# Optimization experiments

Measured on AMD Instinct MI355X. Metric: run time of the kernel, lower is better.

The kernel has to match this reference:

```python
import jax, jax.numpy as jnp
import numpy as np

B, C, HD, H, W = 4, 64, 64, 64, 64  # batch, input_dim, hidden_dim, spatial


def conv1x1(x, w, b):
    # x: [B, Cin, H, W], w: [Cout, Cin], b: [Cout]
    return jnp.einsum('oc,bchw->bohw', w, x) + b[None, :, None, None]


def setup_inputs() -> dict:
    key = jax.random.key(0)
    ks = jax.random.split(key, 16)
    sc = lambda cin: 1.0 / np.sqrt(cin)
    d = {
        'h': jax.random.normal(ks[0], (B, C, H, W), jnp.float32),
        'm': jax.random.normal(ks[1], (B, C, H, W), jnp.float32),
        'Wq': jax.random.normal(ks[2], (HD, C), jnp.float32) * sc(C),
        'bq': jnp.zeros((HD,), jnp.float32),
        'Wk': jax.random.normal(ks[3], (HD, C), jnp.float32) * sc(C),
        'bk': jnp.zeros((HD,), jnp.float32),
        'Wk2': jax.random.normal(ks[4], (HD, C), jnp.float32) * sc(C),
        'bk2': jnp.zeros((HD,), jnp.float32),
        'Wv': jax.random.normal(ks[5], (C, C), jnp.float32) * sc(C),
        'bv': jnp.zeros((C,), jnp.float32),
        'Wv2': jax.random.normal(ks[6], (C, C), jnp.float32) * sc(C),
        'bv2': jnp.zeros((C,), jnp.float32),
        'Wz': jax.random.normal(ks[7], (2 * C, 2 * C), jnp.float32) * sc(2 * C),
        'bz': jnp.zeros((2 * C,), jnp.float32),
        'Wm': jax.random.normal(ks[8], (3 * C, 3 * C), jnp.float32) * sc(3 * C),
        'bm': jnp.zeros((3 * C,), jnp.float32),
    }
    return d


def reference(h, m, Wq, bq, Wk, bk, Wk2, bk2, Wv, bv, Wv2, bv2, Wz, bz, Wm, bm):
    b, c, hh, ww = h.shape
    n = hh * ww
    K_h = conv1x1(h, Wk, bk).reshape(b, HD, n)            # [B, HD, N]
    Q_h = conv1x1(h, Wq, bq).reshape(b, HD, n).transpose(0, 2, 1)  # [B, N, HD]
    V_h = conv1x1(h, Wv, bv).reshape(b, c, n)             # [B, C, N]
    K_m = conv1x1(m, Wk2, bk2).reshape(b, HD, n)
    V_m = conv1x1(m, Wv2, bv2).reshape(b, c, n)

    A_h = jax.nn.softmax(jnp.einsum('bnd,bdk->bnk', Q_h, K_h), axis=-1)  # [B, N, N]
    Z_h = jnp.einsum('bnk,bck->bcn', A_h, V_h).reshape(b, c, hh, ww)
    A_m = jax.nn.softmax(jnp.einsum('bnd,bdk->bnk', Q_h, K_m), axis=-1)
    Z_m = jnp.einsum('bnk,bck->bcn', A_m, V_m).reshape(b, c, hh, ww)

    Z = conv1x1(jnp.concatenate([Z_h, Z_m], axis=1), Wz, bz)   # [B, 2C, H, W]
    combined = conv1x1(jnp.concatenate([Z, h], axis=1), Wm, bm)  # [B, 3C, H, W]
    mo, mg, mi = jnp.split(combined, 3, axis=1)
    mi = jax.nn.sigmoid(mi)
    new_m = (1.0 - mi) * m + mi * jnp.tanh(mg)
    new_h = jax.nn.sigmoid(mo) * new_m
    return (new_h, new_m)
```

## Files before the change

### kernel.cpp

```cpp
#include <hip/hip_runtime.h>

#define BN 4
#define NN 4096
#define SPLITK 2
#define LOG2E 1.44269504f
#define MFIX 36.0f

typedef __attribute__((ext_vector_type(8))) __bf16 bf16x8;
typedef __attribute__((ext_vector_type(4))) short s16x4;
typedef __attribute__((ext_vector_type(4))) float f32x4;
typedef unsigned short u16;

__device__ __forceinline__ u16 f2bf(float x) {
  unsigned int u = __builtin_bit_cast(unsigned int, x);
  u = (u + 0x7fffu + ((u >> 16) & 1u)) >> 16;
  return (u16)u;
}
__device__ __forceinline__ u16 f2bfs(float x) {
  __bf16 b = (__bf16)x;
  return __builtin_bit_cast(u16, b);
}
__device__ __forceinline__ float bf2f(u16 s) {
  unsigned int u = ((unsigned int)s) << 16;
  return __builtin_bit_cast(float, u);
}

__device__ __forceinline__ float fexp2(float x) {
#if defined(__HIP_DEVICE_COMPILE__) && __has_builtin(__builtin_amdgcn_exp2f)
  return __builtin_amdgcn_exp2f(x);
#else
  return __builtin_exp2f(x);
#endif
}

__device__ __forceinline__ f32x4 mfma16(s16x4 a, s16x4 b, f32x4 c) {
#if defined(__HIP_DEVICE_COMPILE__)
  return __builtin_amdgcn_mfma_f32_16x16x16bf16_1k(a, b, c, 0, 0, 0);
#else
  return c;
#endif
}

__device__ __forceinline__ void gld16(const u16* g, u16* l) {
#if defined(__HIP_DEVICE_COMPILE__)
  __builtin_amdgcn_global_load_lds(
      (const __attribute__((address_space(1))) void*)g,
      (__attribute__((address_space(3))) void*)l, 16, 0, 0);
#else
  (void)g; (void)l;
#endif
}

#define PACK16(A, P0, P1)                                                          \
    P0.x = (unsigned)f2bf(A[0]) | ((unsigned)f2bf(A[1]) << 16);                    \
    P0.y = (unsigned)f2bf(A[2]) | ((unsigned)f2bf(A[3]) << 16);                    \
    P0.z = (unsigned)f2bf(A[4]) | ((unsigned)f2bf(A[5]) << 16);                    \
    P0.w = (unsigned)f2bf(A[6]) | ((unsigned)f2bf(A[7]) << 16);                    \
    P1.x = (unsigned)f2bf(A[8]) | ((unsigned)f2bf(A[9]) << 16);                    \
    P1.y = (unsigned)f2bf(A[10]) | ((unsigned)f2bf(A[11]) << 16);                  \
    P1.z = (unsigned)f2bf(A[12]) | ((unsigned)f2bf(A[13]) << 16);                  \
    P1.w = (unsigned)f2bf(A[14]) | ((unsigned)f2bf(A[15]) << 16);

__global__ __launch_bounds__(256) void fuse_w2_kernel(
    const float* __restrict__ Wz, const float* __restrict__ bz,
    const float* __restrict__ Wm, const float* __restrict__ bm,
    u16* __restrict__ Wbig, float* __restrict__ bbig) {
  __shared__ float wrow[128];
  __shared__ float bzs[128];
  int o = blockIdx.x;
  int t = threadIdx.x;
  if (t < 128) { wrow[t] = Wm[o * 192 + t]; bzs[t] = bz[t]; }
  __syncthreads();
  if (t < 128) {
    float s = 0.f;
#pragma unroll 4
    for (int j = 0; j < 128; ++j) s = fmaf(wrow[j], Wz[j * 128 + t], s);
    Wbig[o * 192 + t] = f2bf(s);
  } else if (t < 192) {
    Wbig[o * 192 + t] = f2bf(Wm[o * 192 + t]);
  } else if (t == 192) {
    float s = bm[o];
    for (int j = 0; j < 128; ++j) s = fmaf(wrow[j], bzs[j], s);
    bbig[o] = s;
  }
}

__global__ __launch_bounds__(256) void proj3_kernel(
    const float* __restrict__ h, const float* __restrict__ m,
    const float* __restrict__ Wq, const float* __restrict__ bq,
    const float* __restrict__ Wk, const float* __restrict__ bk,
    const float* __restrict__ Wk2, const float* __restrict__ bk2,
    const float* __restrict__ Wv, const float* __restrict__ bv,
    const float* __restrict__ Wv2, const float* __restrict__ bv2,
    u16* __restrict__ Q, u16* __restrict__ Kh, u16* __restrict__ Km,
    u16* __restrict__ Vh, u16* __restrict__ Vm, u16* __restrict__ hT) {
  __shared__ float xs[64][65];
  __shared__ float Wl[4096];
  int blk = blockIdx.x;
  int ntile = blk & 63, b = (blk >> 6) & 3, pid = blk >> 8;
  int n0 = ntile * 64;
  int t = threadIdx.x, nl = t & 63;
  const float* src = (pid == 2 || pid == 4) ? m : h;
  {
    int c0 = (t >> 6) * 16;
#pragma unroll
    for (int i = 0; i < 16; ++i) {
      int c = c0 + i;
      xs[c][nl] = src[((size_t)(b * 64) + c) * NN + n0 + nl];
    }
  }
  if (pid < 5) {
    const float* W = pid == 0 ? Wq : pid == 1 ? Wk : pid == 2 ? Wk2 : pid == 3 ? Wv : Wv2;
#pragma unroll
    for (int i = 0; i < 16; ++i) Wl[i * 256 + t] = W[i * 256 + t];
  }
  __syncthreads();
  int w = __builtin_amdgcn_readfirstlane(t >> 6);
  size_t nrow = (size_t)b * NN + n0 + nl;
  float acc[16];
  if (pid == 5) {
#pragma unroll
    for (int i = 0; i < 16; ++i) acc[i] = xs[w * 16 + i][nl];
  } else {
    const float* bs = pid == 0 ? bq : pid == 1 ? bk : pid == 2 ? bk2 : pid == 3 ? bv : bv2;
#pragma unroll
    for (int i = 0; i < 16; ++i) acc[i] = bs[w * 16 + i];
    for (int c = 0; c < 64; ++c) {
      float x = xs[c][nl];
#pragma unroll
      for (int i = 0; i < 16; ++i) acc[i] = fmaf(Wl[(w * 16 + i) * 64 + c], x, acc[i]);
    }
    if (pid == 0) {
#pragma unroll
      for (int i = 0; i < 16; ++i) acc[i] *= LOG2E;
    }
  }
  if (pid == 3 || pid == 4) {
    u16* dst = (pid == 3) ? Vh : Vm;
    int key = n0 + nl;
    size_t base = ((size_t)b << 18) + (size_t)(key >> 4) * 1024 + w * 256 +
                  ((key >> 2) & 3) * 64 + (key & 3);
#pragma unroll
    for (int i = 0; i < 16; ++i) dst[base + i * 4] = f2bf(acc[i]);
  } else {
    u16* dst = pid == 0 ? Q : pid == 1 ? Kh : pid == 2 ? Km : hT;
    uint4 p0, p1;
    PACK16(acc, p0, p1);
    uint4* dp = (uint4*)(dst + nrow * 64 + w * 16);
    dp[0] = p0; dp[1] = p1;
  }
}

__global__ __launch_bounds__(256, 2) void flash10_kernel(
    const u16* __restrict__ Qg, const u16* __restrict__ Khg,
    const u16* __restrict__ Kmg, const u16* __restrict__ Vhg,
    const u16* __restrict__ Vmg, u16* __restrict__ Opart,
    float* __restrict__ Lpart) {
  __shared__ u16 Kl[2][8192];
  __shared__ u16 Vl[2][8192];
  int blk = blockIdx.x;
  int combo = blk & 15, qt = blk >> 4;
  int attn = combo & 1, b = (combo >> 1) & 3, split = combo >> 3;
  const u16* K = (attn ? Kmg : Khg) + (size_t)b * NN * 64;
  const u16* V = (attn ? Vmg : Vhg) + ((size_t)b << 18);
  int t = threadIdx.x, wave = t >> 6, lane = t & 63, col = lane & 15, quad = lane >> 4;
  int row0 = qt * 128 + wave * 32;

  bf16x8 bq[2][2];
#pragma unroll
  for (int g = 0; g < 2; ++g) {
    const u16* qp = Qg + (size_t)b * NN * 64 + (size_t)(row0 + g * 16 + col) * 64 + quad * 8;
    bq[g][0] = *(const bf16x8*)(const void*)qp;
    bq[g][1] = *(const bf16x8*)(const void*)(qp + 32);
  }

  f32x4 O[2][4];
#pragma unroll
  for (int g = 0; g < 2; ++g)
#pragma unroll
    for (int i = 0; i < 4; ++i) O[g][i] = f32x4{0.f, 0.f, 0.f, 0.f};
  f32x4 Lacc[2];
  Lacc[0] = f32x4{0.f, 0.f, 0.f, 0.f};
  Lacc[1] = f32x4{0.f, 0.f, 0.f, 0.f};
  const f32x4 minit = {-MFIX, -MFIX, -MFIX, -MFIX};
  s16x4 ones;
#pragma unroll
  for (int i = 0; i < 4; ++i) ones[i] = (short)0x3F80;
  int sp8 = split * 8 + b * 2 + attn;

  const int kbase = split * (NN / SPLITK);
  const int TILES = NN / SPLITK / 128;

#define STAGE(BUF, K0)                                                           \
  _Pragma("unroll") for (int jj = 0; jj < 4; ++jj) {                             \
    int p = jj * 256 + t;                                                        \
    int krow_ = p >> 3;                                                          \
    int kj_ = (p & 7) ^ (krow_ & 7);                                             \
    gld16(K + (size_t)((K0) + krow_) * 64 + kj_ * 8, &Kl[BUF][p * 8]);           \
    gld16(V + (size_t)(K0) * 64 + p * 8, &Vl[BUF][p * 8]);                       \
  }

  STAGE(0, kbase);

  for (int kt = 0; kt < TILES; ++kt) {
    __syncthreads();
    int cur = kt & 1;
    if (kt + 1 < TILES) { STAGE(cur ^ 1, kbase + (kt + 1) * 128); }
    const u16* Kb = &Kl[cur][0];
    const u16* Vb = &Vl[cur][0];
    f32x4 St[8][2];
#pragma unroll
    for (int nt = 0; nt < 8; ++nt) {
      int row = nt * 16 + col;
      int ph0 = row * 8 + (quad ^ (col & 7));
      int ph1 = row * 8 + ((4 + quad) ^ (col & 7));
      bf16x8 a0 = *(const bf16x8*)(const void*)(Kb + ph0 * 8);
      bf16x8 a1 = *(const bf16x8*)(const void*)(Kb + ph1 * 8);
#pragma unroll
      for (int g = 0; g < 2; ++g) {
        f32x4 acc = __builtin_amdgcn_mfma_f32_16x16x32_bf16(a0, bq[g][0], minit, 0, 0, 0);
        acc = __builtin_amdgcn_mfma_f32_16x16x32_bf16(a1, bq[g][1], acc, 0, 0, 0);
        St[nt][g] = acc;
      }
    }
    s16x4 pfrag[8][2];
#pragma unroll
    for (int nt = 0; nt < 8; ++nt)
#pragma unroll
      for (int g = 0; g < 2; ++g) {
        s16x4 pf;
#pragma unroll
        for (int r = 0; r < 4; ++r) pf[r] = (short)f2bfs(fexp2(St[nt][g][r]));
        pfrag[nt][g] = pf;
        Lacc[g] = mfma16(pf, ones, Lacc[g]);
      }
    const u16* vbase = Vb + quad * 64 + col * 4;
#pragma unroll
    for (int nt = 0; nt < 8; ++nt) {
#pragma unroll
      for (int ct = 0; ct < 4; ++ct) {
        s16x4 vf = *(const s16x4*)(const void*)(vbase + nt * 1024 + ct * 256);
        O[0][ct] = mfma16(pfrag[nt][0], vf, O[0][ct]);
        O[1][ct] = mfma16(pfrag[nt][1], vf, O[1][ct]);
      }
    }
  }
#undef STAGE

#pragma unroll
  for (int g = 0; g < 2; ++g) {
#pragma unroll
    for (int ct = 0; ct < 4; ++ct)
#pragma unroll
      for (int r = 0; r < 4; ++r) {
        size_t q = (size_t)row0 + g * 16 + quad * 4 + r;
        Opart[((size_t)sp8 * NN + q) * 64 + ct * 16 + col] = f2bfs(O[g][ct][r]);
      }
    if (col == 0) {
#pragma unroll
      for (int r = 0; r < 4; ++r)
        Lpart[(size_t)sp8 * NN + row0 + g * 16 + quad * 4 + r] = Lacc[g][r];
    }
  }
}

__global__ __launch_bounds__(256) void epi3_kernel(
    const u16* __restrict__ Wb, const float* __restrict__ bb,
    const u16* __restrict__ Opart, const float* __restrict__ Lpart,
    const u16* __restrict__ hT, const float* __restrict__ mglob,
    float* __restrict__ out) {
  int blk = blockIdx.x;
  int ng = blk * 16;
  int b = ng >> 12;
  int t = threadIdx.x, wave = t >> 6, lane = t & 63, col = lane & 15, quad = lane >> 4;
  int qb = (ng & (NN - 1)) + col;
  int s0h = b * 2, s1h = 8 + b * 2, s0m = b * 2 + 1, s1m = 9 + b * 2;
  float invLh = 1.f / (Lpart[(size_t)s0h * NN + qb] + Lpart[(size_t)s1h * NN + qb]);
  float invLm = 1.f / (Lpart[(size_t)s0m * NN + qb] + Lpart[(size_t)s1m * NN + qb]);
  size_t nrow = ((size_t)ng + col) * 64;
  bf16x8 bfr[6];
#define MERGEF(DST, SP0, SP1, OFF, INVL)                                         \
  {                                                                              \
    const u16* p0_ = Opart + ((size_t)(SP0) * NN + qb) * 64 + (OFF);             \
    const u16* p1_ = Opart + ((size_t)(SP1) * NN + qb) * 64 + (OFF);             \
    bf16x8 a_ = *(const bf16x8*)(const void*)p0_;                                \
    bf16x8 c_ = *(const bf16x8*)(const void*)p1_;                                \
    bf16x8 r_;                                                                   \
    _Pragma("unroll") for (int i = 0; i < 8; ++i)                                \
      r_[i] = (__bf16)(((float)a_[i] + (float)c_[i]) * (INVL));                  \
    DST = r_;                                                                    \
  }
  MERGEF(bfr[0], s0h, s1h, quad * 8, invLh);
  MERGEF(bfr[1], s0h, s1h, 32 + quad * 8, invLh);
  MERGEF(bfr[2], s0m, s1m, quad * 8, invLm);
  MERGEF(bfr[3], s0m, s1m, 32 + quad * 8, invLm);
#undef MERGEF
  bfr[4] = *(const bf16x8*)(const void*)(hT + nrow + quad * 8);
  bfr[5] = *(const bf16x8*)(const void*)(hT + nrow + 32 + quad * 8);
  f32x4 acc[3];
#pragma unroll
  for (int j = 0; j < 3; ++j) {
    int mt = wave + j * 4;
#pragma unroll
    for (int r = 0; r < 4; ++r) acc[j][r] = bb[mt * 16 + quad * 4 + r];
  }
#pragma unroll
  for (int ks = 0; ks < 6; ++ks) {
#pragma unroll
    for (int j = 0; j < 3; ++j) {
      int mt = wave + j * 4;
      bf16x8 af = *(const bf16x8*)(const void*)(Wb + (size_t)(mt * 16 + col) * 192 + ks * 32 + quad * 8);
      acc[j] = __builtin_amdgcn_mfma_f32_16x16x32_bf16(af, bfr[ks], acc[j], 0, 0, 0);
    }
  }
  int nloc = (ng & (NN - 1)) + col;
#pragma unroll
  for (int r = 0; r < 4; ++r) {
    int o = wave * 16 + quad * 4 + r;
    float mo = acc[0][r], mgt = acc[1][r], mi = acc[2][r];
    float si = 1.f / (1.f + fexp2(-mi * LOG2E));
    float tg = 1.f - 2.f / (fexp2(2.f * LOG2E * mgt) + 1.f);
    float mv = mglob[(size_t)(b * 64 + o) * NN + nloc];
    float nm = (1.f - si) * mv + si * tg;
    float nh = nm / (1.f + fexp2(-mo * LOG2E));
    out[(size_t)(b * 64 + o) * NN + nloc] = nh;
    out[(size_t)BN * 64 * NN + (size_t)(b * 64 + o) * NN + nloc] = nm;
  }
}

extern "C" void kernel_launch(void* const* d_in, const int* in_sizes, int n_in,
                              void* d_out, int out_size, void* d_ws, size_t ws_size,
                              hipStream_t stream) {
  const float* h = (const float*)d_in[0];
  const float* m = (const float*)d_in[1];
  const float* Wq = (const float*)d_in[2];
  const float* bq = (const float*)d_in[3];
  const float* Wk = (const float*)d_in[4];
  const float* bk = (const float*)d_in[5];
  const float* Wk2 = (const float*)d_in[6];
  const float* bk2 = (const float*)d_in[7];
  const float* Wv = (const float*)d_in[8];
  const float* bv = (const float*)d_in[9];
  const float* Wv2 = (const float*)d_in[10];
  const float* bv2 = (const float*)d_in[11];
  const float* Wz = (const float*)d_in[12];
  const float* bz = (const float*)d_in[13];
  const float* Wm = (const float*)d_in[14];
  const float* bm = (const float*)d_in[15];
  float* out = (float*)d_out;

  size_t off = 0;
  auto alloc = [&](size_t bytes) {
    void* p = (char*)d_ws + off;
    off += (bytes + 255) & ~(size_t)255;
    return p;
  };
  const size_t bn64 = (size_t)BN * NN * 64;
  u16* Q  = (u16*)alloc(bn64 * 2);
  u16* Kh = (u16*)alloc(bn64 * 2);
  u16* Km = (u16*)alloc(bn64 * 2);
  u16* Vh = (u16*)alloc(bn64 * 2);
  u16* Vm = (u16*)alloc(bn64 * 2);
  u16* hT = (u16*)alloc(bn64 * 2);
  u16* Opart = (u16*)alloc((size_t)SPLITK * 8 * NN * 64 * 2);
  float* Lpart = (float*)alloc((size_t)SPLITK * 8 * NN * 4);
  u16* Wbigbf = (u16*)alloc(192 * 192 * 2);
  float* bbig = (float*)alloc(192 * 4);
  (void)ws_size; (void)in_sizes; (void)n_in; (void)out_size;

  fuse_w2_kernel<<<192, 256, 0, stream>>>(Wz, bz, Wm, bm, Wbigbf, bbig);
  proj3_kernel<<<6 * BN * 64, 256, 0, stream>>>(h, m, Wq, bq, Wk, bk, Wk2, bk2, Wv, bv,
                                                Wv2, bv2, Q, Kh, Km, Vh, Vm, hT);
  flash10_kernel<<<512, 256, 0, stream>>>(Q, Kh, Km, Vh, Vm, Opart, Lpart);
  epi3_kernel<<<(BN * NN) / 16, 256, 0, stream>>>(Wbigbf, bbig, Opart, Lpart, hT, m, out);
}
```

Baseline: 175.0 us.

## Use 16x16x32 MFMA for PV, split keys four ways with 64-key tiles

The flash kernel now runs the P·V and row-sum products with the 16x16x32 bf16 MFMA instead of 16x16x16. This needs a new V layout from the projection kernel and a permuted K row order when staging, so two score tiles pack into one 8-wide P fragment. The key dimension is split four ways with 64-key tiles and half the LDS, which doubles the block count and targets 4 blocks per CU, and s_setprio hints are placed around the MFMA phases. The epilogue now sums four partial outputs and normalisers, adding extra partial-buffer traffic and more register pressure under the tighter launch bound.

```diff
diff --git a/kernel.cpp b/kernel.cpp
--- a/kernel.cpp
+++ b/kernel.cpp
@@ -2,12 +2,13 @@
 
 #define BN 4
 #define NN 4096
-#define SPLITK 2
+#define SPLITK 4
+#define KTILE 64
 #define LOG2E 1.44269504f
 #define MFIX 36.0f
 
 typedef __attribute__((ext_vector_type(8))) __bf16 bf16x8;
-typedef __attribute__((ext_vector_type(4))) short s16x4;
+typedef __attribute__((ext_vector_type(8))) short s16x8;
 typedef __attribute__((ext_vector_type(4))) float f32x4;
 typedef unsigned short u16;
 
@@ -19,10 +20,6 @@
 __device__ __forceinline__ u16 f2bfs(float x) {
   __bf16 b = (__bf16)x;
   return __builtin_bit_cast(u16, b);
-}
-__device__ __forceinline__ float bf2f(u16 s) {
-  unsigned int u = ((unsigned int)s) << 16;
-  return __builtin_bit_cast(float, u);
 }
 
 __device__ __forceinline__ float fexp2(float x) {
@@ -33,10 +30,11 @@
 #endif
 }
 
-__device__ __forceinline__ f32x4 mfma16(s16x4 a, s16x4 b, f32x4 c) {
+__device__ __forceinline__ f32x4 mfma32(bf16x8 a, bf16x8 b, f32x4 c) {
 #if defined(__HIP_DEVICE_COMPILE__)
-  return __builtin_amdgcn_mfma_f32_16x16x16bf16_1k(a, b, c, 0, 0, 0);
+  return __builtin_amdgcn_mfma_f32_16x16x32_bf16(a, b, c, 0, 0, 0);
 #else
+  (void)a; (void)b;
   return c;
 #endif
 }
@@ -50,6 +48,12 @@
   (void)g; (void)l;
 #endif
 }
+
+#if defined(__HIP_DEVICE_COMPILE__)
+#define SETPRIO(p) __builtin_amdgcn_s_setprio(p)
+#else
+#define SETPRIO(p)
+#endif
 
 #define PACK16(A, P0, P1)                                                          \
     P0.x = (unsigned)f2bf(A[0]) | ((unsigned)f2bf(A[1]) << 16);                    \
@@ -138,10 +142,10 @@
   if (pid == 3 || pid == 4) {
     u16* dst = (pid == 3) ? Vh : Vm;
     int key = n0 + nl;
-    size_t base = ((size_t)b << 18) + (size_t)(key >> 4) * 1024 + w * 256 +
-                  ((key >> 2) & 3) * 64 + (key & 3);
-#pragma unroll
-    for (int i = 0; i < 16; ++i) dst[base + i * 4] = f2bf(acc[i]);
+    size_t base = ((size_t)b << 18) + (size_t)(key >> 5) * 2048 + w * 512 +
+                  (size_t)((key >> 3) & 3) * 128 + (key & 7);
+#pragma unroll
+    for (int i = 0; i < 16; ++i) dst[base + i * 8] = f2bf(acc[i]);
   } else {
     u16* dst = pid == 0 ? Q : pid == 1 ? Kh : pid == 2 ? Km : hT;
     uint4 p0, p1;
@@ -151,15 +155,15 @@
   }
 }
 
-__global__ __launch_bounds__(256, 2) void flash10_kernel(
+__global__ __launch_bounds__(256, 4) void flash11_kernel(
     const u16* __restrict__ Qg, const u16* __restrict__ Khg,
     const u16* __restrict__ Kmg, const u16* __restrict__ Vhg,
     const u16* __restrict__ Vmg, u16* __restrict__ Opart,
     float* __restrict__ Lpart) {
-  __shared__ u16 Kl[2][8192];
-  __shared__ u16 Vl[2][8192];
+  __shared__ u16 Kl[2][4096];
+  __shared__ u16 Vl[2][4096];
   int blk = blockIdx.x;
-  int combo = blk & 15, qt = blk >> 4;
+  int combo = blk & 31, qt = blk >> 5;
   int attn = combo & 1, b = (combo >> 1) & 3, split = combo >> 3;
   const u16* K = (attn ? Kmg : Khg) + (size_t)b * NN * 64;
   const u16* V = (attn ? Vmg : Vhg) + ((size_t)b << 18);
@@ -183,20 +187,23 @@
   Lacc[0] = f32x4{0.f, 0.f, 0.f, 0.f};
   Lacc[1] = f32x4{0.f, 0.f, 0.f, 0.f};
   const f32x4 minit = {-MFIX, -MFIX, -MFIX, -MFIX};
-  s16x4 ones;
-#pragma unroll
-  for (int i = 0; i < 4; ++i) ones[i] = (short)0x3F80;
-  int sp8 = split * 8 + b * 2 + attn;
+  s16x8 onesv;
+#pragma unroll
+  for (int i = 0; i < 8; ++i) onesv[i] = (short)0x3F80;
+  bf16x8 ones8 = __builtin_bit_cast(bf16x8, onesv);
+  int sp = split * 8 + b * 2 + attn;
 
   const int kbase = split * (NN / SPLITK);
-  const int TILES = NN / SPLITK / 128;
+  const int TILES = NN / SPLITK / KTILE;
 
 #define STAGE(BUF, K0)                                                           \
-  _Pragma("unroll") for (int jj = 0; jj < 4; ++jj) {                             \
+  _Pragma("unroll") for (int jj = 0; jj < 2; ++jj) {                             \
     int p = jj * 256 + t;                                                        \
     int krow_ = p >> 3;                                                          \
     int kj_ = (p & 7) ^ (krow_ & 7);                                             \
-    gld16(K + (size_t)((K0) + krow_) * 64 + kj_ * 8, &Kl[BUF][p * 8]);           \
+    int s5_ = krow_ & 31;                                                        \
+    int tr_ = (krow_ & 32) | ((s5_ & 12) << 1) | (((s5_ >> 4) & 1) << 2) | (s5_ & 3); \
+    gld16(K + (size_t)((K0) + tr_) * 64 + kj_ * 8, &Kl[BUF][p * 8]);             \
     gld16(V + (size_t)(K0) * 64 + p * 8, &Vl[BUF][p * 8]);                       \
   }
 
@@ -205,12 +212,13 @@
   for (int kt = 0; kt < TILES; ++kt) {
     __syncthreads();
     int cur = kt & 1;
-    if (kt + 1 < TILES) { STAGE(cur ^ 1, kbase + (kt + 1) * 128); }
+    if (kt + 1 < TILES) { STAGE(cur ^ 1, kbase + (kt + 1) * KTILE); }
     const u16* Kb = &Kl[cur][0];
     const u16* Vb = &Vl[cur][0];
-    f32x4 St[8][2];
-#pragma unroll
-    for (int nt = 0; nt < 8; ++nt) {
+    f32x4 St[4][2];
+    SETPRIO(1);
+#pragma unroll
+    for (int nt = 0; nt < 4; ++nt) {
       int row = nt * 16 + col;
       int ph0 = row * 8 + (quad ^ (col & 7));
       int ph1 = row * 8 + ((4 + quad) ^ (col & 7));
@@ -218,32 +226,38 @@
       bf16x8 a1 = *(const bf16x8*)(const void*)(Kb + ph1 * 8);
 #pragma unroll
       for (int g = 0; g < 2; ++g) {
-        f32x4 acc = __builtin_amdgcn_mfma_f32_16x16x32_bf16(a0, bq[g][0], minit, 0, 0, 0);
-        acc = __builtin_amdgcn_mfma_f32_16x16x32_bf16(a1, bq[g][1], acc, 0, 0, 0);
+        f32x4 acc = mfma32(a0, bq[g][0], minit);
+        acc = mfma32(a1, bq[g][1], acc);
         St[nt][g] = acc;
       }
     }
-    s16x4 pfrag[8][2];
-#pragma unroll
-    for (int nt = 0; nt < 8; ++nt)
+    SETPRIO(0);
+    bf16x8 pa[2][2];
+#pragma unroll
+    for (int grp = 0; grp < 2; ++grp)
 #pragma unroll
       for (int g = 0; g < 2; ++g) {
-        s16x4 pf;
-#pragma unroll
-        for (int r = 0; r < 4; ++r) pf[r] = (short)f2bfs(fexp2(St[nt][g][r]));
-        pfrag[nt][g] = pf;
-        Lacc[g] = mfma16(pf, ones, Lacc[g]);
+        s16x8 pf;
+#pragma unroll
+        for (int r = 0; r < 4; ++r) {
+          pf[r] = (short)f2bfs(fexp2(St[2 * grp][g][r]));
+          pf[r + 4] = (short)f2bfs(fexp2(St[2 * grp + 1][g][r]));
+        }
+        bf16x8 p8 = __builtin_bit_cast(bf16x8, pf);
+        pa[grp][g] = p8;
+        Lacc[g] = mfma32(p8, ones8, Lacc[g]);
       }
-    const u16* vbase = Vb + quad * 64 + col * 4;
-#pragma unroll
-    for (int nt = 0; nt < 8; ++nt) {
+    const u16* vbase = Vb + lane * 8;
+    SETPRIO(1);
+#pragma unroll
+    for (int grp = 0; grp < 2; ++grp)
 #pragma unroll
       for (int ct = 0; ct < 4; ++ct) {
-        s16x4 vf = *(const s16x4*)(const void*)(vbase + nt * 1024 + ct * 256);
-        O[0][ct] = mfma16(pfrag[nt][0], vf, O[0][ct]);
-        O[1][ct] = mfma16(pfrag[nt][1], vf, O[1][ct]);
+        bf16x8 vf = *(const bf16x8*)(const void*)(vbase + grp * 2048 + ct * 512);
+        O[0][ct] = mfma32(pa[grp][0], vf, O[0][ct]);
+        O[1][ct] = mfma32(pa[grp][1], vf, O[1][ct]);
       }
-    }
+    SETPRIO(0);
   }
 #undef STAGE
 
@@ -254,12 +268,12 @@
 #pragma unroll
       for (int r = 0; r < 4; ++r) {
         size_t q = (size_t)row0 + g * 16 + quad * 4 + r;
-        Opart[((size_t)sp8 * NN + q) * 64 + ct * 16 + col] = f2bfs(O[g][ct][r]);
+        Opart[((size_t)sp * NN + q) * 64 + ct * 16 + col] = f2bfs(O[g][ct][r]);
       }
     if (col == 0) {
 #pragma unroll
       for (int r = 0; r < 4; ++r)
-        Lpart[(size_t)sp8 * NN + row0 + g * 16 + quad * 4 + r] = Lacc[g][r];
+        Lpart[(size_t)sp * NN + row0 + g * 16 + quad * 4 + r] = Lacc[g][r];
     }
   }
 }
@@ -274,26 +288,34 @@
   int b = ng >> 12;
   int t = threadIdx.x, wave = t >> 6, lane = t & 63, col = lane & 15, quad = lane >> 4;
   int qb = (ng & (NN - 1)) + col;
-  int s0h = b * 2, s1h = 8 + b * 2, s0m = b * 2 + 1, s1m = 9 + b * 2;
-  float invLh = 1.f / (Lpart[(size_t)s0h * NN + qb] + Lpart[(size_t)s1h * NN + qb]);
-  float invLm = 1.f / (Lpart[(size_t)s0m * NN + qb] + Lpart[(size_t)s1m * NN + qb]);
+  float Lh = 0.f, Lm = 0.f;
+#pragma unroll
+  for (int s = 0; s < SPLITK; ++s) {
+    Lh += Lpart[(size_t)(s * 8 + b * 2) * NN + qb];
+    Lm += Lpart[(size_t)(s * 8 + b * 2 + 1) * NN + qb];
+  }
+  float invLh = 1.f / Lh;
+  float invLm = 1.f / Lm;
   size_t nrow = ((size_t)ng + col) * 64;
   bf16x8 bfr[6];
-#define MERGEF(DST, SP0, SP1, OFF, INVL)                                         \
+#define MERGEF(DST, ATTN, OFF, INVL)                                             \
   {                                                                              \
-    const u16* p0_ = Opart + ((size_t)(SP0) * NN + qb) * 64 + (OFF);             \
-    const u16* p1_ = Opart + ((size_t)(SP1) * NN + qb) * 64 + (OFF);             \
-    bf16x8 a_ = *(const bf16x8*)(const void*)p0_;                                \
-    bf16x8 c_ = *(const bf16x8*)(const void*)p1_;                                \
+    float s8_[8] = {0.f, 0.f, 0.f, 0.f, 0.f, 0.f, 0.f, 0.f};                     \
+    _Pragma("unroll") for (int sp_ = 0; sp_ < SPLITK; ++sp_) {                   \
+      const u16* p_ =                                                            \
+          Opart + ((size_t)(sp_ * 8 + b * 2 + (ATTN)) * NN + qb) * 64 + (OFF);   \
+      bf16x8 a_ = *(const bf16x8*)(const void*)p_;                               \
+      _Pragma("unroll") for (int i = 0; i < 8; ++i) s8_[i] += (float)a_[i];      \
+    }                                                                            \
     bf16x8 r_;                                                                   \
     _Pragma("unroll") for (int i = 0; i < 8; ++i)                                \
-      r_[i] = (__bf16)(((float)a_[i] + (float)c_[i]) * (INVL));                  \
+      r_[i] = (__bf16)(s8_[i] * (INVL));                                         \
     DST = r_;                                                                    \
   }
-  MERGEF(bfr[0], s0h, s1h, quad * 8, invLh);
-  MERGEF(bfr[1], s0h, s1h, 32 + quad * 8, invLh);
-  MERGEF(bfr[2], s0m, s1m, quad * 8, invLm);
-  MERGEF(bfr[3], s0m, s1m, 32 + quad * 8, invLm);
+  MERGEF(bfr[0], 0, quad * 8, invLh);
+  MERGEF(bfr[1], 0, 32 + quad * 8, invLh);
+  MERGEF(bfr[2], 1, quad * 8, invLm);
+  MERGEF(bfr[3], 1, 32 + quad * 8, invLm);
 #undef MERGEF
   bfr[4] = *(const bf16x8*)(const void*)(hT + nrow + quad * 8);
   bfr[5] = *(const bf16x8*)(const void*)(hT + nrow + 32 + quad * 8);
@@ -310,7 +332,7 @@
     for (int j = 0; j < 3; ++j) {
       int mt = wave + j * 4;
       bf16x8 af = *(const bf16x8*)(const void*)(Wb + (size_t)(mt * 16 + col) * 192 + ks * 32 + quad * 8);
-      acc[j] = __builtin_amdgcn_mfma_f32_16x16x32_bf16(af, bfr[ks], acc[j], 0, 0, 0);
+      acc[j] = mfma32(af, bfr[ks], acc[j]);
     }
   }
   int nloc = (ng & (NN - 1)) + col;
@@ -371,6 +393,6 @@
   fuse_w2_kernel<<<192, 256, 0, stream>>>(Wz, bz, Wm, bm, Wbigbf, bbig);
   proj3_kernel<<<6 * BN * 64, 256, 0, stream>>>(h, m, Wq, bq, Wk, bk, Wk2, bk2, Wv, bv,
                                                 Wv2, bv2, Q, Kh, Km, Vh, Vm, hT);
-  flash10_kernel<<<512, 256, 0, stream>>>(Q, Kh, Km, Vh, Vm, Opart, Lpart);
+  flash11_kernel<<<32 * 32, 256, 0, stream>>>(Q, Kh, Km, Vh, Vm, Opart, Lpart);
   epi3_kernel<<<(BN * NN) / 16, 256, 0, stream>>>(Wbigbf, bbig, Opart, Lpart, hT, m, out);
 }
```

Result: faster. 168.6 us (-3.6%).
